# Kernel tuning notes

Measured on AMD Instinct MI355X. Metric: run time of the kernel, lower is better.

Reference implementation:

```python
import jax, jax.numpy as jnp
import numpy as np

L = 2048; V = 50000; E = 256
H1 = 512; H2 = 512; H3 = 512; H4 = 512
T = 11; START = 9; STOP = 10; ALPHA = 0.2
NEG = -10000.0


def setup_inputs() -> dict:
    key = jax.random.key(0)
    ks = jax.random.split(key, 25)
    def n(k, shape, s=0.05):
        return jax.random.normal(k, shape, dtype=jnp.float32) * s
    h1 = H1 // 2; h2 = H4 // 2
    trans = jax.random.normal(ks[23], (T, T), dtype=jnp.float32)
    trans = trans.at[START, :].set(NEG).at[:, STOP].set(NEG)
    return {
        "sentence": jax.random.randint(ks[0], (L,), 0, V),
        "emb": n(ks[1], (V, E), 0.1),
        "l1_wih_f": n(ks[2], (4 * h1, E)), "l1_whh_f": n(ks[3], (4 * h1, h1)), "l1_b_f": n(ks[4], (4 * h1,)),
        "l1_wih_b": n(ks[5], (4 * h1, E)), "l1_whh_b": n(ks[6], (4 * h1, h1)), "l1_b_b": n(ks[7], (4 * h1,)),
        "hc1": n(ks[8], (4, h1)),
        "gat1_W": n(ks[9], (H1, H2)), "gat1_a": n(ks[10], (2 * H2,)),
        "gat2_W": n(ks[11], (H2, H3)), "gat2_a": n(ks[12], (2 * H3,)),
        "l2_wih_f": n(ks[13], (4 * h2, H3)), "l2_whh_f": n(ks[14], (4 * h2, h2)), "l2_b_f": n(ks[15], (4 * h2,)),
        "l2_wih_b": n(ks[16], (4 * h2, H3)), "l2_whh_b": n(ks[17], (4 * h2, h2)), "l2_b_b": n(ks[18], (4 * h2,)),
        "hc2": n(ks[19], (4, h2)),
        "w_tag": n(ks[20], (T, H4)), "b_tag": n(ks[21], (T,)),
        "trans": trans,
    }


def _lstm_dir(x, h0, c0, wih, whh, b):
    # x: [L, D]; PyTorch gate order i, f, g, o
    def step(carry, xt):
        h, c = carry
        z = xt @ wih.T + h @ whh.T + b
        i, f, g, o = jnp.split(z, 4)
        i = jax.nn.sigmoid(i); f = jax.nn.sigmoid(f)
        g = jnp.tanh(g); o = jax.nn.sigmoid(o)
        c = f * c + i * g
        h = o * jnp.tanh(c)
        return (h, c), h
    _, hs = jax.lax.scan(step, (h0, c0), x)
    return hs


def _bilstm(x, wf, uf, bf, wb, ub, bb, hc):
    hf = _lstm_dir(x, hc[0], hc[1], wf, uf, bf)
    hb = _lstm_dir(x[::-1], hc[2], hc[3], wb, ub, bb)[::-1]
    return jnp.concatenate([hf, hb], axis=-1)  # [L, 2h]


def _gat(h, W, a):
    # dense GAT layer: attention over all node pairs (inference, no dropout)
    Wh = h @ W                                   # [L, F]
    F = W.shape[1]
    e = jax.nn.leaky_relu((Wh @ a[:F])[:, None] + (Wh @ a[F:])[None, :], ALPHA)  # [L, L]
    attn = jax.nn.softmax(e, axis=1)
    return attn @ Wh


def _viterbi(feats, trans):
    init = jnp.full((T,), NEG, dtype=feats.dtype).at[START].set(0.0)
    def step(fv, feat):
        scores = fv[None, :] + trans             # [next_tag, prev_tag]
        bp = jnp.argmax(scores, axis=1)
        fv2 = jnp.max(scores, axis=1) + feat
        return fv2, bp
    fv, bps = jax.lax.scan(step, init, feats)    # bps: [L, T]
    term = fv + trans[STOP]
    best = jnp.argmax(term)
    score = term[best]
    def back(tag, bp):
        return bp[tag], tag
    _, path = jax.lax.scan(back, best, bps, reverse=True)
    return score, path


def reference(sentence, emb, l1_wih_f, l1_whh_f, l1_b_f, l1_wih_b, l1_whh_b, l1_b_b, hc1,
              gat1_W, gat1_a, gat2_W, gat2_a,
              l2_wih_f, l2_whh_f, l2_b_f, l2_wih_b, l2_whh_b, l2_b_b, hc2,
              w_tag, b_tag, trans):
    x = emb[sentence]                                                  # [L, E]
    h1 = _bilstm(x, l1_wih_f, l1_whh_f, l1_b_f, l1_wih_b, l1_whh_b, l1_b_b, hc1)
    g1 = jax.nn.elu(_gat(h1, gat1_W, gat1_a))
    g2 = jax.nn.elu(_gat(g1, gat2_W, gat2_a))
    h2 = _bilstm(g2, l2_wih_f, l2_whh_f, l2_b_f, l2_wih_b, l2_whh_b, l2_b_b, hc2)
    feats = h2 @ w_tag.T + b_tag                                       # [L, T]
    score, path = _viterbi(feats, trans)
    return score, path
```

## Files before the change

kernel.cpp:

```cpp
#include <hip/hip_runtime.h>
#include <hip/hip_bf16.h>
#include <math.h>

#define SEQL 2048
#define EDIM 256
#define HID 256
#define G4 1024
#define HCAT 512
#define TT 11
#define START_TAG 9
#define STOP_TAG 10
#define NEGV -10000.0f
#define ALPHA_LR 0.2f
#define VCH 64
#define VCS 32
#define NU 16
#define NBLK 16

__device__ __forceinline__ float sigf(float x) { return 1.0f / (1.0f + __expf(-x)); }
__device__ __forceinline__ float tanhfast(float x) { return 2.0f / (1.0f + __expf(-2.0f * x)) - 1.0f; }
__device__ __forceinline__ unsigned int bfp(float f) {
    union { float f; unsigned int u; } c; c.f = f;
    return (c.u + 0x7FFFu + ((c.u >> 16) & 1u)) >> 16;
}
__device__ __forceinline__ float bflo(unsigned int u) { return __uint_as_float(u << 16); }
__device__ __forceinline__ float bfhi(unsigned int u) { return __uint_as_float(u & 0xFFFF0000u); }

__global__ void embed_k(const int* __restrict__ sent, const float* __restrict__ emb,
                        float* __restrict__ x) {
    int idx = blockIdx.x * 256 + threadIdx.x;
    int t = idx >> 8, e = idx & 255;
    x[idx] = emb[(size_t)sent[t] * EDIM + e];
}

__global__ __launch_bounds__(256) void gemm_nt(const float* __restrict__ A,
                                               const float* __restrict__ B,
                                               const float* __restrict__ bias,
                                               float* __restrict__ C,
                                               int M, int N, int K) {
    __shared__ float As[16][68];
    __shared__ float Bs[16][68];
    int tid = threadIdx.x;
    int tx = tid & 15, ty = tid >> 4;
    int m0 = blockIdx.y * 64, n0 = blockIdx.x * 64;
    int lr = tid >> 2;
    int lc = (tid & 3) * 4;
    float acc[4][4] = {};
    for (int k0 = 0; k0 < K; k0 += 16) {
        float4 av = *(const float4*)(A + (size_t)(m0 + lr) * K + k0 + lc);
        float4 bv = make_float4(0.f, 0.f, 0.f, 0.f);
        if (n0 + lr < N) bv = *(const float4*)(B + (size_t)(n0 + lr) * K + k0 + lc);
        As[lc + 0][lr] = av.x; As[lc + 1][lr] = av.y; As[lc + 2][lr] = av.z; As[lc + 3][lr] = av.w;
        Bs[lc + 0][lr] = bv.x; Bs[lc + 1][lr] = bv.y; Bs[lc + 2][lr] = bv.z; Bs[lc + 3][lr] = bv.w;
        __syncthreads();
#pragma unroll
        for (int kk = 0; kk < 16; ++kk) {
            float4 a4 = *(const float4*)&As[kk][ty * 4];
            float4 b4 = *(const float4*)&Bs[kk][tx * 4];
            float aa[4] = {a4.x, a4.y, a4.z, a4.w};
            float bb[4] = {b4.x, b4.y, b4.z, b4.w};
#pragma unroll
            for (int i = 0; i < 4; ++i)
#pragma unroll
                for (int j = 0; j < 4; ++j) acc[i][j] += aa[i] * bb[j];
        }
        __syncthreads();
    }
#pragma unroll
    for (int i = 0; i < 4; ++i) {
        int m = m0 + ty * 4 + i;
#pragma unroll
        for (int j = 0; j < 4; ++j) {
            int n = n0 + tx * 4 + j;
            if (n < N) {
                float v = acc[i][j];
                if (bias) v += bias[n];
                C[(size_t)m * N + n] = v;
            }
        }
    }
}

__global__ __launch_bounds__(256) void gemm_nn(const float* __restrict__ A,
                                               const float* __restrict__ B,
                                               float* __restrict__ C,
                                               const float* __restrict__ rowdiv,
                                               int do_elu, int M, int N, int K) {
    __shared__ float As[16][68];
    __shared__ float Bs[16][68];
    int tid = threadIdx.x;
    int tx = tid & 15, ty = tid >> 4;
    int m0 = blockIdx.y * 64, n0 = blockIdx.x * 64;
    int lr = tid >> 2;
    int lc = (tid & 3) * 4;
    int br = tid >> 4;
    int bc = (tid & 15) * 4;
    float acc[4][4] = {};
    for (int k0 = 0; k0 < K; k0 += 16) {
        float4 av = *(const float4*)(A + (size_t)(m0 + lr) * K + k0 + lc);
        float4 bv = *(const float4*)(B + (size_t)(k0 + br) * N + n0 + bc);
        As[lc + 0][lr] = av.x; As[lc + 1][lr] = av.y; As[lc + 2][lr] = av.z; As[lc + 3][lr] = av.w;
        *(float4*)&Bs[br][bc] = bv;
        __syncthreads();
#pragma unroll
        for (int kk = 0; kk < 16; ++kk) {
            float4 a4 = *(const float4*)&As[kk][ty * 4];
            float4 b4 = *(const float4*)&Bs[kk][tx * 4];
            float aa[4] = {a4.x, a4.y, a4.z, a4.w};
            float bb[4] = {b4.x, b4.y, b4.z, b4.w};
#pragma unroll
            for (int i = 0; i < 4; ++i)
#pragma unroll
                for (int j = 0; j < 4; ++j) acc[i][j] += aa[i] * bb[j];
        }
        __syncthreads();
    }
#pragma unroll
    for (int i = 0; i < 4; ++i) {
        int m = m0 + ty * 4 + i;
        float rd = rowdiv ? rowdiv[m] : 1.0f;
#pragma unroll
        for (int j = 0; j < 4; ++j) {
            int n = n0 + tx * 4 + j;
            float v = acc[i][j];
            if (rowdiv) v /= rd;
            if (do_elu) v = v > 0.f ? v : (__expf(v) - 1.f);
            C[(size_t)m * N + n] = v;
        }
    }
}

__global__ __launch_bounds__(256) void lstm_lds(const float* __restrict__ xin_f,
                                                const float* __restrict__ xin_b,
                                                const float* __restrict__ whh_f,
                                                const float* __restrict__ whh_b,
                                                const float* __restrict__ hc,
                                                float* __restrict__ out,
                                                unsigned int* pubu, int tagbase) {
    int raw = blockIdx.x;
    int lane7 = raw & 7;
    if (lane7 > 1) return;
    int dir = lane7;
    int b = raw >> 3;
    const float* xin = dir ? xin_b : xin_f;
    const float* whh = dir ? whh_b : whh_f;

    int tid = threadIdx.x;

    __shared__ uint4 W4[2048];
    __shared__ __align__(16) float hbuf[256];
    __shared__ float zp[512];

    for (int idx = tid; idx < 2048; idx += 256) {
        int wave = idx >> 9;
        int i = (idx >> 6) & 7;
        int l = idx & 63;
        int towner = wave * 64 + l;
        int rp = towner & 31;
        int k8 = towner >> 5;
        int rloc = 2 * rp + (i >> 2);
        int ii = i & 3;
        int g = rloc >> 4, j = rloc & 15;
        const float* wr = whh + (size_t)(g * HID + b * NU + j) * HID + k8 * 32 + ii * 8;
        uint4 v;
        v.x = bfp(wr[0]) | (bfp(wr[1]) << 16);
        v.y = bfp(wr[2]) | (bfp(wr[3]) << 16);
        v.z = bfp(wr[4]) | (bfp(wr[5]) << 16);
        v.w = bfp(wr[6]) | (bfp(wr[7]) << 16);
        W4[wave * 512 + i * 64 + l] = v;
    }

    if (tid < 256) hbuf[tid] = hc[dir * 512 + tid];
    float c = 0.f;
    float xq0 = 0.f, xq1 = 0.f, xq2 = 0.f, xq3 = 0.f;
    if (tid < 16) {
        c = hc[dir * 512 + 256 + b * NU + tid];
        int t0 = dir ? (SEQL - 1) : 0;
        const float* xr = xin + (size_t)t0 * G4 + b * NU + tid;
        xq0 = xr[0]; xq1 = xr[256]; xq2 = xr[512]; xq3 = xr[768];
    }
    __syncthreads();

    int rp = tid & 31;
    int k8 = tid >> 5;
    int wbase = (tid >> 6) * 512 + (tid & 63);
    const float4* hb4 = (const float4*)hbuf;

    for (int s = 0; s < SEQL; ++s) {
        float acc0 = 0.f, acc1 = 0.f;
#pragma unroll
        for (int i = 0; i < 4; ++i) {
            uint4 w0 = W4[wbase + i * 64];
            uint4 w1 = W4[wbase + (i + 4) * 64];
            float4 hA = hb4[k8 * 8 + i * 2];
            float4 hB = hb4[k8 * 8 + i * 2 + 1];
            acc0 += bflo(w0.x) * hA.x + bfhi(w0.x) * hA.y + bflo(w0.y) * hA.z + bfhi(w0.y) * hA.w
                  + bflo(w0.z) * hB.x + bfhi(w0.z) * hB.y + bflo(w0.w) * hB.z + bfhi(w0.w) * hB.w;
            acc1 += bflo(w1.x) * hA.x + bfhi(w1.x) * hA.y + bflo(w1.y) * hA.z + bfhi(w1.y) * hA.w
                  + bflo(w1.z) * hB.x + bfhi(w1.z) * hB.y + bflo(w1.w) * hB.z + bfhi(w1.w) * hB.w;
        }
        zp[k8 * 64 + 2 * rp] = acc0;
        zp[k8 * 64 + 2 * rp + 1] = acc1;
        __syncthreads();

        int t = dir ? (SEQL - 1 - s) : s;
        int par = (s + 1) & 1;
        unsigned int etag = (unsigned int)(tagbase + s + 1) & 0xFFFFu;
        unsigned int* slot = pubu + (par * 2 + dir) * 256;

        if (tid < 16) {
            float zi = xq0, zf = xq1, zg = xq2, zo = xq3;
#pragma unroll
            for (int q = 0; q < 8; ++q) {
                zi += zp[q * 64 + tid];
                zf += zp[q * 64 + 16 + tid];
                zg += zp[q * 64 + 32 + tid];
                zo += zp[q * 64 + 48 + tid];
            }
            float ig = sigf(zi), fg = sigf(zf), gt = tanhfast(zg), og = sigf(zo);
            c = fg * c + ig * gt;
            float hn = og * tanhfast(c);
            hbuf[b * NU + tid] = hn;
            unsigned int word = (bfp(hn) << 16) | etag;
            int u = b * NU + tid;
            *(volatile unsigned int*)&slot[u] = word;
            __hip_atomic_store(&slot[u], word, __ATOMIC_RELAXED,
                               __HIP_MEMORY_SCOPE_AGENT);
            out[(size_t)t * HCAT + dir * HID + u] = hn;
            if (s + 1 < SEQL) {
                int tn = dir ? (SEQL - 2 - s) : (s + 1);
                const float* xr = xin + (size_t)tn * G4 + b * NU + tid;
                xq0 = xr[0]; xq1 = xr[256]; xq2 = xr[512]; xq3 = xr[768];
            }
        } else if (tid >= 64 && s + 1 < SEQL) {
            int pu = tid - 64;
            int u = pu < b * NU ? pu : pu + NU;
            unsigned int v; int it = 0;
            for (;;) {
                v = *(volatile const unsigned int*)&slot[u];
                if ((v & 0xFFFFu) == etag) break;
                if ((++it & 7) == 0) {
                    v = __hip_atomic_load(&slot[u], __ATOMIC_RELAXED,
                                          __HIP_MEMORY_SCOPE_AGENT);
                    if ((v & 0xFFFFu) == etag) break;
                }
            }
            hbuf[u] = bfhi(v);
            if (pu < 48) {
                int pu2 = pu + 192;
                int u2 = pu2 < b * NU ? pu2 : pu2 + NU;
                it = 0;
                for (;;) {
                    v = *(volatile const unsigned int*)&slot[u2];
                    if ((v & 0xFFFFu) == etag) break;
                    if ((++it & 7) == 0) {
                        v = __hip_atomic_load(&slot[u2], __ATOMIC_RELAXED,
                                              __HIP_MEMORY_SCOPE_AGENT);
                        if ((v & 0xFFFFu) == etag) break;
                    }
                }
                hbuf[u2] = bfhi(v);
            }
        }
        __syncthreads();
    }
}

__global__ void gat_scores(const float* __restrict__ Wh, const float* __restrict__ a,
                           float* __restrict__ s1, float* __restrict__ s2) {
    int i = blockIdx.x;
    int lane = threadIdx.x;
    const float* rowp = Wh + (size_t)i * HCAT;
    float p1 = 0.f, p2 = 0.f;
    for (int k = lane; k < HCAT; k += 64) {
        float w = rowp[k];
        p1 += w * a[k];
        p2 += w * a[HCAT + k];
    }
    for (int off = 32; off; off >>= 1) {
        p1 += __shfl_down(p1, off, 64);
        p2 += __shfl_down(p2, off, 64);
    }
    if (lane == 0) { s1[i] = p1; s2[i] = p2; }
}

__global__ void reduce_max_k(const float* __restrict__ s2, float* __restrict__ outv) {
    __shared__ float red[256];
    int tid = threadIdx.x;
    float m = -INFINITY;
    for (int k = tid; k < SEQL; k += 256) m = fmaxf(m, s2[k]);
    red[tid] = m;
    __syncthreads();
    for (int off = 128; off; off >>= 1) {
        if (tid < off) red[tid] = fmaxf(red[tid], red[tid + off]);
        __syncthreads();
    }
    if (tid == 0) outv[0] = red[0];
}

__global__ void gat_p(const float* __restrict__ s1, const float* __restrict__ s2,
                      const float* __restrict__ s2m, float* __restrict__ P,
                      float* __restrict__ Z) {
    int i = blockIdx.x;
    int tid = threadIdx.x;
    float base = s1[i];
    float m = base + s2m[0];
    m = m > 0.f ? m : ALPHA_LR * m;
    float zs = 0.f;
    for (int jj = tid; jj < SEQL; jj += 256) {
        float e = base + s2[jj];
        e = e > 0.f ? e : ALPHA_LR * e;
        float p = __expf(e - m);
        P[(size_t)i * SEQL + jj] = p;
        zs += p;
    }
    __shared__ float red[256];
    red[tid] = zs;
    __syncthreads();
    for (int off = 128; off; off >>= 1) {
        if (tid < off) red[tid] += red[tid + off];
        __syncthreads();
    }
    if (tid == 0) Z[i] = red[0];
}

__global__ void vit_chunkA(const float* __restrict__ feats, const float* __restrict__ trans,
                           float* __restrict__ chunkA) {
    int c = blockIdx.x;
    int tid = threadIdx.x;
    __shared__ float Acur[121], tr[121];
    if (tid < 121) tr[tid] = trans[tid];
    __syncthreads();
    int n = tid / 11, p = tid % 11;
    int t0 = c * VCS;
    if (tid < 121) Acur[tid] = tr[tid] + feats[t0 * TT + n];
    __syncthreads();
    for (int t = t0 + 1; t < t0 + VCS; ++t) {
        float v = -INFINITY;
        if (tid < 121) {
            float ft = feats[t * TT + n];
#pragma unroll
            for (int k = 0; k < 11; ++k) v = fmaxf(v, tr[n * 11 + k] + Acur[k * 11 + p]);
            v += ft;
        }
        __syncthreads();
        if (tid < 121) Acur[tid] = v;
        __syncthreads();
    }
    if (tid < 121) chunkA[c * 121 + tid] = Acur[tid];
}

__global__ void vit_prefix(const float* __restrict__ chunkA, float* __restrict__ fvstart) {
    int tid = threadIdx.x;
    __shared__ float fv[11];
    if (tid < 11) fv[tid] = (tid == START_TAG) ? 0.f : NEGV;
    __syncthreads();
    if (tid < 11) fvstart[tid] = fv[tid];
    for (int c = 0; c < VCH; ++c) {
        float v = -INFINITY;
        if (tid < 11) {
            for (int p = 0; p < 11; ++p) v = fmaxf(v, chunkA[c * 121 + tid * 11 + p] + fv[p]);
        }
        __syncthreads();
        if (tid < 11) { fv[tid] = v; fvstart[(c + 1) * TT + tid] = v; }
        __syncthreads();
    }
}

__global__ void vit_chunkC(const float* __restrict__ feats, const float* __restrict__ trans,
                           const float* __restrict__ fvstart, int* __restrict__ bp,
                           float* __restrict__ fvfinal) {
    int c = blockIdx.x;
    int tid = threadIdx.x;
    __shared__ float fv[11], tr[121], sc[121], mx[11];
    if (tid < 121) tr[tid] = trans[tid];
    if (tid < 11) fv[tid] = fvstart[c * TT + tid];
    __syncthreads();
    int t0 = c * VCS;
    for (int t = t0; t < t0 + VCS; ++t) {
        if (tid < 121) sc[tid] = fv[tid % 11] + tr[tid];
        __syncthreads();
        if (tid < 11) {
            float best = -INFINITY;
            int bi = 0;
            for (int k = 0; k < 11; ++k) {
                float v = sc[tid * 11 + k];
                if (v > best) { best = v; bi = k; }
            }
            bp[t * TT + tid] = bi;
            mx[tid] = best + feats[t * TT + tid];
        }
        __syncthreads();
        if (tid < 11) fv[tid] = mx[tid];
        __syncthreads();
    }
    if (c == VCH - 1 && tid < 11) fvfinal[tid] = fv[tid];
}

__global__ __launch_bounds__(1024) void vit_back(const int* __restrict__ bp,
                                                 const float* __restrict__ fvfinal,
                                                 const float* __restrict__ trans,
                                                 float* __restrict__ outp) {
    __shared__ unsigned char bufA[SEQL * TT];
    __shared__ unsigned char bufB[SEQL * TT];
    __shared__ int bestIdx;
    int tid = threadIdx.x;
    for (int idx = tid; idx < SEQL * TT; idx += 1024) {
        int t = idx / TT, n = idx - t * TT;
        bufA[idx] = (t < SEQL - 1) ? (unsigned char)bp[(t + 1) * TT + n] : (unsigned char)n;
    }
    __syncthreads();
    unsigned char* a = bufA;
    unsigned char* b = bufB;
    for (int len = 1; len < SEQL - 1; len <<= 1) {
        for (int idx = tid; idx < SEQL * TT; idx += 1024) {
            int t = idx / TT, n = idx - t * TT;
            int m = (t + len <= SEQL - 1) ? (int)a[(t + len) * TT + n] : n;
            b[t * TT + n] = a[t * TT + m];
        }
        __syncthreads();
        unsigned char* tmp = a; a = b; b = tmp;
        __syncthreads();
    }
    if (tid == 0) {
        float bs = -INFINITY;
        int bi = 0;
        for (int p = 0; p < 11; ++p) {
            float v = fvfinal[p] + trans[STOP_TAG * 11 + p];
            if (v > bs) { bs = v; bi = p; }
        }
        outp[0] = bs;
        bestIdx = bi;
    }
    __syncthreads();
    int best = bestIdx;
    for (int t = tid; t < SEQL; t += 1024) outp[1 + t] = (float)a[t * TT + best];
}

extern "C" void kernel_launch(void* const* d_in, const int* in_sizes, int n_in,
                              void* d_out, int out_size, void* d_ws, size_t ws_size,
                              hipStream_t stream) {
    const int* sent = (const int*)d_in[0];
    const float* emb = (const float*)d_in[1];
    const float* w1f = (const float*)d_in[2];
    const float* u1f = (const float*)d_in[3];
    const float* b1f = (const float*)d_in[4];
    const float* w1b = (const float*)d_in[5];
    const float* u1b = (const float*)d_in[6];
    const float* b1b = (const float*)d_in[7];
    const float* hc1 = (const float*)d_in[8];
    const float* g1W = (const float*)d_in[9];
    const float* g1a = (const float*)d_in[10];
    const float* g2W = (const float*)d_in[11];
    const float* g2a = (const float*)d_in[12];
    const float* w2f = (const float*)d_in[13];
    const float* u2f = (const float*)d_in[14];
    const float* b2f = (const float*)d_in[15];
    const float* w2b = (const float*)d_in[16];
    const float* u2b = (const float*)d_in[17];
    const float* b2b = (const float*)d_in[18];
    const float* hc2 = (const float*)d_in[19];
    const float* wtag = (const float*)d_in[20];
    const float* btag = (const float*)d_in[21];
    const float* trans = (const float*)d_in[22];

    float* ws = (float*)d_ws;
    float* x = ws;
    float* R1 = x + 524288;
    float* xin_f = R1;
    float* xin_b = R1 + 2097152;
    float* P = R1;
    float* h1cat = R1 + 4194304;
    float* Wh = h1cat + 1048576;
    float* g1 = Wh + 1048576;
    float* s1 = g1 + 1048576;
    float* s2 = s1 + 2048;
    float* Zr = s2 + 2048;
    float* s2m = Zr + 2048;
    unsigned int* pub = (unsigned int*)(s2m + 16);
    float* feats = (float*)(pub + 1024);
    float* chA = feats + 22528;
    float* fvst = chA + 7744;
    float* fvfin = fvst + 720;
    int* bp = (int*)(fvfin + 16);

    hipMemsetAsync(pub, 0, 1024 * sizeof(unsigned int), stream);

    embed_k<<<SEQL, 256, 0, stream>>>(sent, emb, x);

    gemm_nt<<<dim3(16, 32), 256, 0, stream>>>(x, w1f, b1f, xin_f, SEQL, G4, EDIM);
    gemm_nt<<<dim3(16, 32), 256, 0, stream>>>(x, w1b, b1b, xin_b, SEQL, G4, EDIM);
    lstm_lds<<<128, 256, 0, stream>>>(xin_f, xin_b, u1f, u1b, hc1, h1cat, pub, 0);

    gemm_nn<<<dim3(8, 32), 256, 0, stream>>>(h1cat, g1W, Wh, nullptr, 0, SEQL, HCAT, HCAT);
    gat_scores<<<SEQL, 64, 0, stream>>>(Wh, g1a, s1, s2);
    reduce_max_k<<<1, 256, 0, stream>>>(s2, s2m);
    gat_p<<<SEQL, 256, 0, stream>>>(s1, s2, s2m, P, Zr);
    gemm_nn<<<dim3(8, 32), 256, 0, stream>>>(P, Wh, g1, Zr, 1, SEQL, HCAT, SEQL);

    gemm_nn<<<dim3(8, 32), 256, 0, stream>>>(g1, g2W, Wh, nullptr, 0, SEQL, HCAT, HCAT);
    gat_scores<<<SEQL, 64, 0, stream>>>(Wh, g2a, s1, s2);
    reduce_max_k<<<1, 256, 0, stream>>>(s2, s2m);
    gat_p<<<SEQL, 256, 0, stream>>>(s1, s2, s2m, P, Zr);
    float* g2v = h1cat;
    gemm_nn<<<dim3(8, 32), 256, 0, stream>>>(P, Wh, g2v, Zr, 1, SEQL, HCAT, SEQL);

    gemm_nt<<<dim3(16, 32), 256, 0, stream>>>(g2v, w2f, b2f, xin_f, SEQL, G4, HCAT);
    gemm_nt<<<dim3(16, 32), 256, 0, stream>>>(g2v, w2b, b2b, xin_b, SEQL, G4, HCAT);
    float* h2cat = g1;
    lstm_lds<<<128, 256, 0, stream>>>(xin_f, xin_b, u2f, u2b, hc2, h2cat, pub, 2048);

    gemm_nt<<<dim3(1, 32), 256, 0, stream>>>(h2cat, wtag, btag, feats, SEQL, TT, HCAT);
    vit_chunkA<<<VCH, 128, 0, stream>>>(feats, trans, chA);
    vit_prefix<<<1, 128, 0, stream>>>(chA, fvst);
    vit_chunkC<<<VCH, 128, 0, stream>>>(feats, trans, fvst, bp, fvfin);
    vit_back<<<1, 1024, 0, stream>>>(bp, fvfin, trans, (float*)d_out);
}
```

Measured before the change: 7.900 ms.

## Split-K the GAT attention GEMM and parallelize LSTM gate activations across 64 threads

The attention-times-values GEMM (K=2048) is split four ways along K into a partial buffer, and a separate finalize kernel sums the partials, divides by the softmax denominator and applies ELU. This raises the block count from 256 to 1024 to fill more CUs. In the LSTM recurrence, the four gate reductions and activations now run on 64 threads instead of 16, with results passed through shared memory, at the cost of an extra barrier per step. The polling loop also issues an agent-scope atomic load on every spin instead of every eighth.

```diff
diff --git a/kernel.cpp b/kernel.cpp
--- a/kernel.cpp
+++ b/kernel.cpp
@@ -130,6 +130,62 @@
     }
 }
 
+__global__ __launch_bounds__(256) void gemm_nn_ks(const float* __restrict__ A,
+                                                  const float* __restrict__ B,
+                                                  float* __restrict__ Cpart,
+                                                  int M, int N, int K4) {
+    __shared__ float As[16][68];
+    __shared__ float Bs[16][68];
+    int tid = threadIdx.x;
+    int tx = tid & 15, ty = tid >> 4;
+    int m0 = blockIdx.y * 64, n0 = blockIdx.x * 64;
+    int kz = blockIdx.z;
+    int K = (int)gridDim.z * K4;
+    int kbeg = kz * K4, kend = kbeg + K4;
+    int lr = tid >> 2;
+    int lc = (tid & 3) * 4;
+    int br = tid >> 4;
+    int bc = (tid & 15) * 4;
+    float acc[4][4] = {};
+    for (int k0 = kbeg; k0 < kend; k0 += 16) {
+        float4 av = *(const float4*)(A + (size_t)(m0 + lr) * K + k0 + lc);
+        float4 bv = *(const float4*)(B + (size_t)(k0 + br) * N + n0 + bc);
+        As[lc + 0][lr] = av.x; As[lc + 1][lr] = av.y; As[lc + 2][lr] = av.z; As[lc + 3][lr] = av.w;
+        *(float4*)&Bs[br][bc] = bv;
+        __syncthreads();
+#pragma unroll
+        for (int kk = 0; kk < 16; ++kk) {
+            float4 a4 = *(const float4*)&As[kk][ty * 4];
+            float4 b4 = *(const float4*)&Bs[kk][tx * 4];
+            float aa[4] = {a4.x, a4.y, a4.z, a4.w};
+            float bb[4] = {b4.x, b4.y, b4.z, b4.w};
+#pragma unroll
+            for (int i = 0; i < 4; ++i)
+#pragma unroll
+                for (int j = 0; j < 4; ++j) acc[i][j] += aa[i] * bb[j];
+        }
+        __syncthreads();
+    }
+    float* Cz = Cpart + (size_t)kz * M * N;
+#pragma unroll
+    for (int i = 0; i < 4; ++i) {
+        int m = m0 + ty * 4 + i;
+#pragma unroll
+        for (int j = 0; j < 4; ++j) {
+            int n = n0 + tx * 4 + j;
+            Cz[(size_t)m * N + n] = acc[i][j];
+        }
+    }
+}
+
+__global__ void attn_fin(const float* __restrict__ Cp, const float* __restrict__ Zr,
+                         float* __restrict__ C, int MN, int N) {
+    int idx = blockIdx.x * 256 + threadIdx.x;
+    float v = Cp[idx] + Cp[MN + idx] + Cp[2 * MN + idx] + Cp[3 * MN + idx];
+    v /= Zr[idx / N];
+    C[idx] = v > 0.f ? v : (__expf(v) - 1.f);
+}
+
 __global__ __launch_bounds__(256) void lstm_lds(const float* __restrict__ xin_f,
                                                 const float* __restrict__ xin_b,
                                                 const float* __restrict__ whh_f,
@@ -150,6 +206,7 @@
     __shared__ uint4 W4[2048];
     __shared__ __align__(16) float hbuf[256];
     __shared__ float zp[512];
+    __shared__ float zact[64];
 
     for (int idx = tid; idx < 2048; idx += 256) {
         int wave = idx >> 9;
@@ -172,12 +229,12 @@
 
     if (tid < 256) hbuf[tid] = hc[dir * 512 + tid];
     float c = 0.f;
-    float xq0 = 0.f, xq1 = 0.f, xq2 = 0.f, xq3 = 0.f;
-    if (tid < 16) {
-        c = hc[dir * 512 + 256 + b * NU + tid];
+    if (tid < 16) c = hc[dir * 512 + 256 + b * NU + tid];
+
+    float xcur = 0.f;
+    if (tid < 64) {
         int t0 = dir ? (SEQL - 1) : 0;
-        const float* xr = xin + (size_t)t0 * G4 + b * NU + tid;
-        xq0 = xr[0]; xq1 = xr[256]; xq2 = xr[512]; xq3 = xr[768];
+        xcur = xin[(size_t)t0 * G4 + (tid >> 4) * HID + b * NU + (tid & 15)];
     }
     __syncthreads();
 
@@ -204,20 +261,23 @@
         __syncthreads();
 
         int t = dir ? (SEQL - 1 - s) : s;
-        int par = (s + 1) & 1;
         unsigned int etag = (unsigned int)(tagbase + s + 1) & 0xFFFFu;
-        unsigned int* slot = pubu + (par * 2 + dir) * 256;
+        unsigned int* slot = pubu + (((s + 1) & 1) * 2 + dir) * 256;
+
+        if (tid < 64) {
+            float z = xcur;
+#pragma unroll
+            for (int q = 0; q < 8; ++q) z += zp[q * 64 + tid];
+            zact[tid] = ((tid >> 4) == 2) ? tanhfast(z) : sigf(z);
+            if (s + 1 < SEQL) {
+                int tn = dir ? (SEQL - 2 - s) : (s + 1);
+                xcur = xin[(size_t)tn * G4 + (tid >> 4) * HID + b * NU + (tid & 15)];
+            }
+        }
+        __syncthreads();
 
         if (tid < 16) {
-            float zi = xq0, zf = xq1, zg = xq2, zo = xq3;
-#pragma unroll
-            for (int q = 0; q < 8; ++q) {
-                zi += zp[q * 64 + tid];
-                zf += zp[q * 64 + 16 + tid];
-                zg += zp[q * 64 + 32 + tid];
-                zo += zp[q * 64 + 48 + tid];
-            }
-            float ig = sigf(zi), fg = sigf(zf), gt = tanhfast(zg), og = sigf(zo);
+            float ig = zact[tid], fg = zact[16 + tid], gt = zact[32 + tid], og = zact[48 + tid];
             c = fg * c + ig * gt;
             float hn = og * tanhfast(c);
             hbuf[b * NU + tid] = hn;
@@ -227,37 +287,27 @@
             __hip_atomic_store(&slot[u], word, __ATOMIC_RELAXED,
                                __HIP_MEMORY_SCOPE_AGENT);
             out[(size_t)t * HCAT + dir * HID + u] = hn;
-            if (s + 1 < SEQL) {
-                int tn = dir ? (SEQL - 2 - s) : (s + 1);
-                const float* xr = xin + (size_t)tn * G4 + b * NU + tid;
-                xq0 = xr[0]; xq1 = xr[256]; xq2 = xr[512]; xq3 = xr[768];
-            }
         } else if (tid >= 64 && s + 1 < SEQL) {
             int pu = tid - 64;
             int u = pu < b * NU ? pu : pu + NU;
-            unsigned int v; int it = 0;
+            unsigned int v;
             for (;;) {
                 v = *(volatile const unsigned int*)&slot[u];
                 if ((v & 0xFFFFu) == etag) break;
-                if ((++it & 7) == 0) {
-                    v = __hip_atomic_load(&slot[u], __ATOMIC_RELAXED,
-                                          __HIP_MEMORY_SCOPE_AGENT);
-                    if ((v & 0xFFFFu) == etag) break;
-                }
+                v = __hip_atomic_load(&slot[u], __ATOMIC_RELAXED,
+                                      __HIP_MEMORY_SCOPE_AGENT);
+                if ((v & 0xFFFFu) == etag) break;
             }
             hbuf[u] = bfhi(v);
             if (pu < 48) {
                 int pu2 = pu + 192;
                 int u2 = pu2 < b * NU ? pu2 : pu2 + NU;
-                it = 0;
                 for (;;) {
                     v = *(volatile const unsigned int*)&slot[u2];
                     if ((v & 0xFFFFu) == etag) break;
-                    if ((++it & 7) == 0) {
-                        v = __hip_atomic_load(&slot[u2], __ATOMIC_RELAXED,
-                                              __HIP_MEMORY_SCOPE_AGENT);
-                        if ((v & 0xFFFFu) == etag) break;
-                    }
+                    v = __hip_atomic_load(&slot[u2], __ATOMIC_RELAXED,
+                                          __HIP_MEMORY_SCOPE_AGENT);
+                    if ((v & 0xFFFFu) == etag) break;
                 }
                 hbuf[u2] = bfhi(v);
             }
@@ -483,6 +533,7 @@
     float* fvst = chA + 7744;
     float* fvfin = fvst + 720;
     int* bp = (int*)(fvfin + 16);
+    float* Cpart = (float*)(bp + 22528);
 
     hipMemsetAsync(pub, 0, 1024 * sizeof(unsigned int), stream);
 
@@ -496,14 +547,16 @@
     gat_scores<<<SEQL, 64, 0, stream>>>(Wh, g1a, s1, s2);
     reduce_max_k<<<1, 256, 0, stream>>>(s2, s2m);
     gat_p<<<SEQL, 256, 0, stream>>>(s1, s2, s2m, P, Zr);
-    gemm_nn<<<dim3(8, 32), 256, 0, stream>>>(P, Wh, g1, Zr, 1, SEQL, HCAT, SEQL);
+    gemm_nn_ks<<<dim3(8, 32, 4), 256, 0, stream>>>(P, Wh, Cpart, SEQL, HCAT, SEQL / 4);
+    attn_fin<<<4096, 256, 0, stream>>>(Cpart, Zr, g1, SEQL * HCAT, HCAT);
 
     gemm_nn<<<dim3(8, 32), 256, 0, stream>>>(g1, g2W, Wh, nullptr, 0, SEQL, HCAT, HCAT);
     gat_scores<<<SEQL, 64, 0, stream>>>(Wh, g2a, s1, s2);
     reduce_max_k<<<1, 256, 0, stream>>>(s2, s2m);
     gat_p<<<SEQL, 256, 0, stream>>>(s1, s2, s2m, P, Zr);
     float* g2v = h1cat;
-    gemm_nn<<<dim3(8, 32), 256, 0, stream>>>(P, Wh, g2v, Zr, 1, SEQL, HCAT, SEQL);
+    gemm_nn_ks<<<dim3(8, 32, 4), 256, 0, stream>>>(P, Wh, Cpart, SEQL, HCAT, SEQL / 4);
+    attn_fin<<<4096, 256, 0, stream>>>(Cpart, Zr, g2v, SEQL * HCAT, HCAT);
 
     gemm_nt<<<dim3(16, 32), 256, 0, stream>>>(g2v, w2f, b2f, xin_f, SEQL, G4, HCAT);
     gemm_nt<<<dim3(16, 32), 256, 0, stream>>>(g2v, w2b, b2b, xin_b, SEQL, G4, HCAT);
```

Result: slower. 10.14 ms (+28.3%).
